# Kernel tuning notes

Hardware: AMD Instinct MI355X
Metric: run time of the kernel (lower is better)

The kernel has to match this reference:

```python
import jax, jax.numpy as jnp
import numpy as np

B, N, DIM = 4, 4096, 768
H = 12
DH = DIM // H          # 64
S = 16                 # num_segments
M = N // S             # 256 segment_len
SCALE = DH ** -0.5


def setup_inputs() -> dict:
    key = jax.random.key(0)
    ks = jax.random.split(key, 7)
    std = DIM ** -0.5
    return {
        "x": jax.random.normal(ks[0], (B, N, DIM), dtype=jnp.float32),
        "Wq": jax.random.normal(ks[1], (DIM, DIM), dtype=jnp.float32) * std,
        "Wkv": jax.random.normal(ks[2], (DIM, DIM), dtype=jnp.float32) * std,
        "Wo": jax.random.normal(ks[3], (DIM, DIM), dtype=jnp.float32) * std,
        "bo": jax.random.normal(ks[4], (DIM,), dtype=jnp.float32) * 0.02,
        "Wo0": jax.random.normal(ks[5], (DIM, DIM), dtype=jnp.float32) * std,
        "bo0": jax.random.normal(ks[6], (DIM,), dtype=jnp.float32) * 0.02,
    }


def _rotary_freqs(n, dh, dtype):
    # lucidrains RotaryEmbedding: inv_freq over even dims, emb = cat(freqs, freqs)
    inv_freq = 1.0 / (10000.0 ** (jnp.arange(0, dh, 2, dtype=jnp.float32) / dh))
    t = jnp.arange(n, dtype=jnp.float32)
    freqs = jnp.einsum("n,f->nf", t, inv_freq)           # (n, dh/2)
    return jnp.concatenate([freqs, freqs], axis=-1).astype(dtype)  # (n, dh)


def _rotate_half(t):
    # '... (j d) -> ... j d', j=2 ; (-x2, x1)
    x1, x2 = jnp.split(t, 2, axis=-1)
    return jnp.concatenate([-x2, x1], axis=-1)


def _apply_rotary(freqs, t):
    # freqs: (1, n, dh) broadcast over (bh, n, dh); rot_dim == dh here
    return t * jnp.cos(freqs) + _rotate_half(t) * jnp.sin(freqs)


def reference(x, Wq, Wkv, Wo, bo, Wo0, bo0):
    b, n, dim = x.shape
    q = x @ Wq            # (b, n, dim), bias-free
    kv = x @ Wkv          # shared K==V projection

    def to_heads(t):      # 'b n (h d) -> (b h) n d'
        return t.reshape(b, n, H, DH).transpose(0, 2, 1, 3).reshape(b * H, n, DH)

    q, kv = to_heads(q), to_heads(kv)

    freqs = _rotary_freqs(n, DH, x.dtype)[None, :, :]    # (1, n, dh)
    q = _apply_rotary(freqs, q)
    kv = _apply_rotary(freqs, kv)

    q = q * SCALE
    c = b * H
    qs = q.reshape(c, S, M, DH)
    kvs = kv.reshape(c, S, M, DH)

    # adjacent-segment KV windows: segment t attends to [t-1, t] for t>=1
    kvs_ccs = jnp.concatenate([kvs[:, :-1], kvs[:, 1:]], axis=2)  # (c, S-1, 2M, dh)
    qs_ccs = qs[:, 1:]                                            # (c, S-1, M, dh)

    lsim = jnp.einsum("csmd,csnd->csmn", qs_ccs, kvs_ccs)         # (c, S-1, M, 2M)
    attn1 = jax.nn.softmax(lsim, axis=-1)
    out1 = jnp.einsum("csmn,csnd->csmd", attn1, kvs_ccs)          # (c, S-1, M, dh)

    # global (self) attention within first segment
    q0, kv0 = qs[:, 0], kvs[:, 0]                                 # (c, M, dh)
    sim0 = jnp.einsum("cmd,cnd->cmn", q0, kv0)
    attn0 = jax.nn.softmax(sim0, axis=-1)
    out0 = jnp.einsum("cmn,cnd->cmd", attn0, kv0)                 # (c, M, dh)

    def merge_heads(t, nn):  # '(b h) nn d -> b nn (h d)'
        return t.reshape(b, H, nn, DH).transpose(0, 2, 1, 3).reshape(b, nn, H * DH)

    out_1 = merge_heads(out1.reshape(c, (S - 1) * M, DH), (S - 1) * M)
    out_0 = merge_heads(out0, M)

    out_1o = out_1 @ Wo + bo
    out_0o = out_0 @ Wo0 + bo0
    return jnp.concatenate([out_0o, out_1o], axis=1)              # (b, n, dim)
```

## Files before the change

kernel.cpp:

```cpp
#include <hip/hip_runtime.h>
#include <hip/hip_bf16.h>


typedef float f32x4 __attribute__((ext_vector_type(4)));
typedef short bf16x8 __attribute__((ext_vector_type(8)));

#define DEV static __device__ __forceinline__

DEV short f2bf(float f) {
  union { __hip_bfloat16 h; unsigned short u; } cv;
  cv.h = __float2bfloat16(f);
  return (short)cv.u;
}

DEV f32x4 fz4() { f32x4 z = {0.f, 0.f, 0.f, 0.f}; return z; }

DEV void gload16(const void* g, void* l) {
  __builtin_amdgcn_global_load_lds((const __attribute__((address_space(1))) void*)g,
                                   (__attribute__((address_space(3))) void*)l, 16, 0, 0);
}

__global__ void __launch_bounds__(256) k_rope(float* __restrict__ cosT,
                                              float* __restrict__ sinT) {
  int idx = blockIdx.x * 256 + threadIdx.x;
  int pos = idx >> 5, jm = idx & 31;
  float invf = exp2f(-(float)jm * (13.287712379549449f / 32.0f));
  float th = (float)pos * invf;
  cosT[idx] = cosf(th);
  sinT[idx] = sinf(th);
}

__global__ void __launch_bounds__(256) k_cvtx(const float* __restrict__ x,
                                              short* __restrict__ xb) {
  int i = (blockIdx.x * 256 + threadIdx.x) * 8;
  float4 a = *(const float4*)(x + i);
  float4 b = *(const float4*)(x + i + 4);
  bf16x8 v;
  v[0] = f2bf(a.x); v[1] = f2bf(a.y); v[2] = f2bf(a.z); v[3] = f2bf(a.w);
  v[4] = f2bf(b.x); v[5] = f2bf(b.y); v[6] = f2bf(b.z); v[7] = f2bf(b.w);
  *(bf16x8*)(xb + i) = v;
}

__global__ void __launch_bounds__(256) k_transw(const float* __restrict__ Wq,
                                                const float* __restrict__ Wkv,
                                                const float* __restrict__ Wo,
                                                const float* __restrict__ Wo0,
                                                short* __restrict__ WtQKV,
                                                short* __restrict__ WtO) {
  __shared__ float t[64][65];
  int z = blockIdx.z;
  const float* src = (z == 0) ? Wq : (z == 1) ? Wkv : (z == 2) ? Wo : Wo0;
  short* dst = (z < 2) ? (WtQKV + (size_t)z * (768 * 768))
                       : (WtO + (size_t)(z - 2) * (768 * 768));
  int k0 = blockIdx.x * 64, j0 = blockIdx.y * 64;
  int tc = threadIdx.x & 63, tr = threadIdx.x >> 6;
#pragma unroll
  for (int i = 0; i < 16; i++) {
    int r = i * 4 + tr;
    t[tc][r] = src[(size_t)(k0 + r) * 768 + j0 + tc];
  }
  __syncthreads();
#pragma unroll
  for (int i = 0; i < 16; i++) {
    int r = i * 4 + tr;
    dst[(size_t)(j0 + r) * 768 + k0 + tc] = f2bf(t[r][tc]);
  }
}

#define QSTAGE(Abuf, Bbuf, Abase, Bbase, kt)                                   \
  {                                                                            \
    _Pragma("unroll") for (int i = 0; i < 2; i++) {                            \
      int rowi = i * 64 + wid * 16 + (lane >> 2);                              \
      int cci = (kt) * 64 + ((((lane & 3) ^ (rowi & 3)) << 4));                \
      gload16((Abase) + (size_t)(r0 + rowi) * 1536 + cci,                      \
              (char*)(Abuf) + i * 4096 + wid * 1024);                          \
      gload16((Bbase) + (size_t)(j0 + rowi) * 1536 + cci,                      \
              (char*)(Bbuf) + i * 4096 + wid * 1024);                          \
    }                                                                          \
  }

__global__ void __launch_bounds__(256, 4) k_gemm_qkv(
    const short* __restrict__ xb, const short* __restrict__ Wt,
    const float* __restrict__ cosT, const float* __restrict__ sinT,
    short* __restrict__ Qb, short* __restrict__ KVb) {
  __shared__ short Al[2][4096];
  __shared__ short Bl[2][4096];
  int bid = blockIdx.x;
  int xcd = bid & 7, loc = bid >> 3;
  int r0 = (xcd * 16 + loc / 12) * 128;
  int cbk = loc % 12;
  bool isQ = cbk < 6;
  int cbl = isQ ? cbk : cbk - 6;
  const char* Ab = (const char*)xb;
  const char* Bb = (const char*)(Wt + (isQ ? (size_t)0 : (size_t)(768 * 768)));
  int j0 = cbl * 128;
  int tid = threadIdx.x, lane = tid & 63, wid = tid >> 6;
  int wr = wid >> 1, wc = wid & 1;
  int l15 = lane & 15, lg = lane >> 4;
  int rsw = (l15 & 3) << 4;

  f32x4 acc[4][4];
#pragma unroll
  for (int i = 0; i < 4; i++)
#pragma unroll
    for (int j = 0; j < 4; j++) acc[i][j] = fz4();

  QSTAGE(Al[0], Bl[0], Ab, Bb, 0)
  for (int kt = 0; kt < 24; kt++) {
    int cb = kt & 1;
    __syncthreads();
    if (kt + 1 < 24) QSTAGE(Al[cb ^ 1], Bl[cb ^ 1], Ab, Bb, kt + 1)
    const char* Ac = (const char*)Al[cb];
    const char* Bc = (const char*)Bl[cb];
    bf16x8 af[4], bfr[4];
#pragma unroll
    for (int mr = 0; mr < 4; mr++)
      af[mr] = *(const bf16x8*)(Ac + (wr * 64 + mr * 16 + l15) * 64 + ((lg * 16) ^ rsw));
#pragma unroll
    for (int nc = 0; nc < 4; nc++)
      bfr[nc] = *(const bf16x8*)(Bc + (wc * 64 + nc * 16 + l15) * 64 + ((lg * 16) ^ rsw));
#pragma unroll
    for (int mr = 0; mr < 4; mr++)
#pragma unroll
      for (int nc = 0; nc < 4; nc++)
        acc[mr][nc] = __builtin_amdgcn_mfma_f32_16x16x32_bf16(af[mr], bfr[nc], acc[mr][nc], 0, 0, 0);
  }

  int h = 2 * cbl + wc;
  short* Ob = isQ ? Qb : KVb;
  float scl = isQ ? 0.18033688011112042f : 1.0f;
#pragma unroll
  for (int mr = 0; mr < 4; mr++) {
#pragma unroll
    for (int rg = 0; rg < 4; rg++) {
      int r = r0 + wr * 64 + mr * 16 + lg * 4 + rg;
      int b = r >> 12, pos = r & 4095;
      const float* cT = cosT + pos * 32;
      const float* sT = sinT + pos * 32;
      float c0 = cT[l15], s0 = sT[l15];
      float c1 = cT[16 + l15], s1 = sT[16 + l15];
      float v0 = acc[mr][0][rg], v1 = acc[mr][1][rg];
      float v2 = acc[mr][2][rg], v3 = acc[mr][3][rg];
      size_t base = ((size_t)((b * 12 + h) * 4096 + pos)) * 64 + l15;
      Ob[base]      = f2bf((v0 * c0 - v2 * s0) * scl);
      Ob[base + 16] = f2bf((v1 * c1 - v3 * s1) * scl);
      Ob[base + 32] = f2bf((v2 * c0 + v0 * s0) * scl);
      Ob[base + 48] = f2bf((v3 * c1 + v1 * s1) * scl);
    }
  }
}

__global__ void __launch_bounds__(256) k_transkv(const short* __restrict__ KVb,
                                                 short* __restrict__ KVt) {
  __shared__ short T[64][72];
  int c = blockIdx.x;
  int pt = blockIdx.y;
  int t = threadIdx.x;
  int ch = t & 7, rr = t >> 3;
#pragma unroll
  for (int i = 0; i < 2; i++) {
    int p = rr + i * 32;
    bf16x8 v = *(const bf16x8*)&KVb[((size_t)c * 4096 + pt * 64 + p) * 64 + ch * 8];
    *(bf16x8*)&T[p][ch * 8] = v;
  }
  __syncthreads();
#pragma unroll
  for (int i = 0; i < 2; i++) {
    int d = rr + i * 32;
    bf16x8 v;
#pragma unroll
    for (int j = 0; j < 8; j++) {
      int cc = ch * 8 + j;
      int g = cc >> 5, sig = cc & 31;
      int p = g * 32 + 4 * (sig >> 3) + (sig & 3) + 16 * ((sig >> 2) & 1);
      v[j] = T[p][d];
    }
    *(bf16x8*)&KVt[((size_t)c * 64 + d) * 4096 + pt * 64 + ch * 8] = v;
  }
}

#define STAGE(buf, kk0)                                                        \
  {                                                                            \
    _Pragma("unroll") for (int i = 0; i < 2; i++) {                            \
      gload16(KVc + (size_t)((kk0) + i * 32 + krow) * 128 + ksrccol,           \
              (char*)Kl[buf] + i * 4096 + wid * 1024);                         \
      gload16(KVtc + ((size_t)(i * 32 + krow) * 4096 + (kk0)) * 2 + ksrccol,   \
              (char*)Vl[buf] + i * 4096 + wid * 1024);                         \
    }                                                                          \
  }

__global__ void __launch_bounds__(256, 4) k_attn(const short* __restrict__ Qb,
                                                 const short* __restrict__ KVbp,
                                                 const short* __restrict__ KVtp,
                                                 short* __restrict__ AO) {
  __shared__ short Kl[2][4096];
  __shared__ short Vl[2][4096];
  int bid = blockIdx.x;
  int orig = (bid & 7) * 192 + (bid >> 3);
  int c = orig >> 5;
  int e = orig & 31;
  int s = (e < 2) ? 0 : ((e - 2) >> 1) + 1;
  int qh = (e < 2) ? e : (e - 2) & 1;
  int NC = (s == 0) ? 4 : 8;
  int Kbase = (s == 0) ? 0 : (s - 1) * 256;

  int tid = threadIdx.x, lane = tid & 63, wid = tid >> 6;
  int l15 = lane & 15, lg = lane >> 4;
  const char* KVc = (const char*)(KVbp + (size_t)c * 4096 * 64);
  const char* KVtc = (const char*)(KVtp + (size_t)c * 64 * 4096);

  int krow = tid >> 3;
  int ksrccol = ((tid & 7) * 16) ^ ((krow & 7) << 4);
  int swz = (l15 & 7) << 4;

  int q0 = s * 256 + qh * 128 + wid * 32;
  bf16x8 qf[2][2];
#pragma unroll
  for (int qt = 0; qt < 2; qt++) {
    const short* Qr = Qb + ((size_t)c * 4096 + q0 + qt * 16 + l15) * 64 + lg * 8;
    qf[qt][0] = *(const bf16x8*)Qr;
    qf[qt][1] = *(const bf16x8*)(Qr + 32);
  }

  const f32x4 mi = {-32.f, -32.f, -32.f, -32.f};
  bf16x8 ones;
#pragma unroll
  for (int j = 0; j < 8; j++) ones[j] = (short)0x3F80;

  f32x4 oacc[2][4];
  f32x4 lacc[2];
#pragma unroll
  for (int qt = 0; qt < 2; qt++) {
    lacc[qt] = fz4();
#pragma unroll
    for (int vt = 0; vt < 4; vt++) oacc[qt][vt] = fz4();
  }

  STAGE(0, Kbase)
  for (int ch = 0; ch < NC; ch++) {
    int cb = ch & 1;
    __syncthreads();
    if (ch + 1 < NC) STAGE(cb ^ 1, Kbase + (ch + 1) * 64)
    const char* Kb_ = (const char*)Kl[cb];
    const char* Vb_ = (const char*)Vl[cb];
#pragma unroll
    for (int u = 0; u < 2; u++) {
      f32x4 z[2][2];
#pragma unroll
      for (int t2 = 0; t2 < 2; t2++) {
        const char* Kp = Kb_ + ((2 * u + t2) * 16 + l15) * 128;
        bf16x8 kf0 = *(const bf16x8*)(Kp + ((lg * 16) ^ swz));
        bf16x8 kf1 = *(const bf16x8*)(Kp + ((64 + lg * 16) ^ swz));
        __builtin_amdgcn_s_setprio(1);
#pragma unroll
        for (int qt = 0; qt < 2; qt++) {
          f32x4 zz = __builtin_amdgcn_mfma_f32_16x16x32_bf16(kf0, qf[qt][0], mi, 0, 0, 0);
          zz = __builtin_amdgcn_mfma_f32_16x16x32_bf16(kf1, qf[qt][1], zz, 0, 0, 0);
          z[qt][t2] = zz;
        }
        __builtin_amdgcn_s_setprio(0);
      }
      bf16x8 pf[2];
#pragma unroll
      for (int qt = 0; qt < 2; qt++) {
#pragma unroll
        for (int t2 = 0; t2 < 2; t2++)
#pragma unroll
          for (int r = 0; r < 4; r++)
            pf[qt][t2 * 4 + r] = f2bf(exp2f(z[qt][t2][r]));
      }
      bf16x8 vf[4];
#pragma unroll
      for (int vt = 0; vt < 4; vt++)
        vf[vt] = *(const bf16x8*)(Vb_ + (vt * 16 + l15) * 128 +
                                  ((u * 64 + lg * 16) ^ swz));
      __builtin_amdgcn_s_setprio(1);
#pragma unroll
      for (int qt = 0; qt < 2; qt++) {
#pragma unroll
        for (int vt = 0; vt < 4; vt++)
          oacc[qt][vt] = __builtin_amdgcn_mfma_f32_16x16x32_bf16(pf[qt], vf[vt], oacc[qt][vt], 0, 0, 0);
        lacc[qt] = __builtin_amdgcn_mfma_f32_16x16x32_bf16(pf[qt], ones, lacc[qt], 0, 0, 0);
      }
      __builtin_amdgcn_s_setprio(0);
    }
  }

  int bq = c / 12, hh = c % 12;
#pragma unroll
  for (int qt = 0; qt < 2; qt++) {
    float rinv[4];
#pragma unroll
    for (int r = 0; r < 4; r++) rinv[r] = 1.0f / lacc[qt][r];
#pragma unroll
    for (int vt = 0; vt < 4; vt++)
#pragma unroll
      for (int r = 0; r < 4; r++) {
        size_t row = (size_t)bq * 4096 + q0 + qt * 16 + lg * 4 + r;
        AO[row * 768 + hh * 64 + vt * 16 + l15] = f2bf(oacc[qt][vt][r] * rinv[r]);
      }
  }
}

__global__ void __launch_bounds__(256, 4) k_gemm_out(
    const short* __restrict__ AO, const short* __restrict__ Wt,
    const float* __restrict__ bo, const float* __restrict__ bo0,
    float* __restrict__ out) {
  __shared__ short Al[2][4096];
  __shared__ short Bl[2][4096];
  int bid = blockIdx.x;
  int xcd = bid & 7, loc = bid >> 3;
  int r0 = (xcd * 16 + loc / 6) * 128;
  int j0 = (loc % 6) * 128;
  bool o0sel = (r0 & 4095) < 256;
  const char* Ab = (const char*)AO;
  const char* Bb = (const char*)(Wt + (o0sel ? (size_t)1 : (size_t)0) * (768 * 768));
  const float* bias = o0sel ? bo0 : bo;
  int tid = threadIdx.x, lane = tid & 63, wid = tid >> 6;
  int wr = wid >> 1, wc = wid & 1;
  int l15 = lane & 15, lg = lane >> 4;
  int rsw = (l15 & 3) << 4;

  f32x4 acc[4][4];
#pragma unroll
  for (int i = 0; i < 4; i++)
#pragma unroll
    for (int j = 0; j < 4; j++) acc[i][j] = fz4();

  QSTAGE(Al[0], Bl[0], Ab, Bb, 0)
  for (int kt = 0; kt < 24; kt++) {
    int cb = kt & 1;
    __syncthreads();
    if (kt + 1 < 24) QSTAGE(Al[cb ^ 1], Bl[cb ^ 1], Ab, Bb, kt + 1)
    const char* Ac = (const char*)Al[cb];
    const char* Bc = (const char*)Bl[cb];
    bf16x8 af[4], bfr[4];
#pragma unroll
    for (int mr = 0; mr < 4; mr++)
      af[mr] = *(const bf16x8*)(Ac + (wr * 64 + mr * 16 + l15) * 64 + ((lg * 16) ^ rsw));
#pragma unroll
    for (int nc = 0; nc < 4; nc++)
      bfr[nc] = *(const bf16x8*)(Bc + (wc * 64 + nc * 16 + l15) * 64 + ((lg * 16) ^ rsw));
#pragma unroll
    for (int mr = 0; mr < 4; mr++)
#pragma unroll
      for (int nc = 0; nc < 4; nc++)
        acc[mr][nc] = __builtin_amdgcn_mfma_f32_16x16x32_bf16(af[mr], bfr[nc], acc[mr][nc], 0, 0, 0);
  }

  float bs[4];
#pragma unroll
  for (int nc = 0; nc < 4; nc++) bs[nc] = bias[j0 + wc * 64 + nc * 16 + l15];
#pragma unroll
  for (int mr = 0; mr < 4; mr++)
#pragma unroll
    for (int rg = 0; rg < 4; rg++) {
      size_t r = (size_t)r0 + wr * 64 + mr * 16 + lg * 4 + rg;
      float* op = out + r * 768 + j0 + wc * 64 + l15;
      op[0]  = acc[mr][0][rg] + bs[0];
      op[16] = acc[mr][1][rg] + bs[1];
      op[32] = acc[mr][2][rg] + bs[2];
      op[48] = acc[mr][3][rg] + bs[3];
    }
}

extern "C" void kernel_launch(void* const* d_in, const int* in_sizes, int n_in,
                              void* d_out, int out_size, void* d_ws, size_t ws_size,
                              hipStream_t stream) {
  (void)in_sizes; (void)n_in; (void)out_size; (void)ws_size;
  const float* x   = (const float*)d_in[0];
  const float* Wq  = (const float*)d_in[1];
  const float* Wkv = (const float*)d_in[2];
  const float* Wo  = (const float*)d_in[3];
  const float* bo  = (const float*)d_in[4];
  const float* Wo0 = (const float*)d_in[5];
  const float* bo0 = (const float*)d_in[6];
  float* out = (float*)d_out;

  char* ws = (char*)d_ws;
  short* xb    = (short*)(ws + 0);
  short* AO    = xb;
  short* Qb    = (short*)(ws + 25165824);
  short* KVb   = (short*)(ws + 50331648);
  short* KVt   = (short*)(ws + 75497472);
  short* WtQKV = (short*)(ws + 75497472);
  float* cosT  = (float*)(ws + 77856768);
  float* sinT  = (float*)(ws + 78381056);
  short* WtO   = (short*)(ws + 100663296);

  k_rope<<<512, 256, 0, stream>>>(cosT, sinT);
  k_cvtx<<<6144, 256, 0, stream>>>(x, xb);
  k_transw<<<dim3(12, 12, 4), 256, 0, stream>>>(Wq, Wkv, Wo, Wo0, WtQKV, WtO);
  k_gemm_qkv<<<1536, 256, 0, stream>>>(xb, WtQKV, cosT, sinT, Qb, KVb);
  k_transkv<<<dim3(48, 64), 256, 0, stream>>>(KVb, KVt);
  k_attn<<<1536, 256, 0, stream>>>(Qb, KVb, KVt, AO);
  k_gemm_out<<<768, 256, 0, stream>>>(AO, WtO, bo, bo0, out);
}
```

Measured before the change: 156.5 us.

## Use a four-stage LDS ring with explicit vmcnt waits in projection GEMMs

Replaces the double-buffered k-loop in the QKV and output projection GEMMs with a 4-slot shared-memory ring that prefetches two k-steps ahead. It uses explicit s_waitcnt vmcnt counts and a raw s_barrier instead of __syncthreads. The goal is to hide global-to-LDS load latency behind MFMA work. In exchange, LDS use rises to 64KB per block and launch bounds drop from 4 to 2 blocks per CU, which lowers occupancy.

```diff
diff --git a/kernel.cpp b/kernel.cpp
--- a/kernel.cpp
+++ b/kernel.cpp
@@ -67,24 +67,55 @@
   }
 }
 
-#define QSTAGE(Abuf, Bbuf, Abase, Bbase, kt)                                   \
+#define STAGE32(Lbuf, Abase, Bbase, s)                                         \
   {                                                                            \
     _Pragma("unroll") for (int i = 0; i < 2; i++) {                            \
-      int rowi = i * 64 + wid * 16 + (lane >> 2);                              \
-      int cci = (kt) * 64 + ((((lane & 3) ^ (rowi & 3)) << 4));                \
-      gload16((Abase) + (size_t)(r0 + rowi) * 1536 + cci,                      \
-              (char*)(Abuf) + i * 4096 + wid * 1024);                          \
-      gload16((Bbase) + (size_t)(j0 + rowi) * 1536 + cci,                      \
-              (char*)(Bbuf) + i * 4096 + wid * 1024);                          \
+      int ch_ = i * 256 + tid;                                                 \
+      int row_ = ch_ >> 2, c_ = ch_ & 3;                                       \
+      int col_ = (s) * 64 + ((c_ ^ (row_ & 3)) << 4);                          \
+      gload16((Abase) + (size_t)(r0 + row_) * 1536 + col_,                     \
+              (char*)(Lbuf) + i * 4096 + wid * 1024);                          \
+      gload16((Bbase) + (size_t)(j0 + row_) * 1536 + col_,                     \
+              (char*)(Lbuf) + 8192 + i * 4096 + wid * 1024);                   \
     }                                                                          \
   }
 
-__global__ void __launch_bounds__(256, 4) k_gemm_qkv(
+#define RING_KLOOP(LQ, Ab, Bb, BODY)                                           \
+  STAGE32(LQ[0], Ab, Bb, 0)                                                    \
+  STAGE32(LQ[1], Ab, Bb, 1)                                                    \
+  for (int s = 0; s < 24; s++) {                                               \
+    if (s < 22) {                                                              \
+      STAGE32(LQ[(s + 2) & 3], Ab, Bb, s + 2)                                  \
+      asm volatile("s_waitcnt vmcnt(8)" ::: "memory");                         \
+    } else if (s == 22) {                                                      \
+      asm volatile("s_waitcnt vmcnt(4)" ::: "memory");                         \
+    } else {                                                                   \
+      asm volatile("s_waitcnt vmcnt(0)" ::: "memory");                         \
+    }                                                                          \
+    __builtin_amdgcn_sched_barrier(0);                                         \
+    __builtin_amdgcn_s_barrier();                                              \
+    __builtin_amdgcn_sched_barrier(0);                                         \
+    const char* Ac = (const char*)LQ[s & 3];                                   \
+    const char* Bc = Ac + 8192;                                                \
+    bf16x8 af[4], bfr[4];                                                      \
+    _Pragma("unroll") for (int mr = 0; mr < 4; mr++)                           \
+        af[mr] = *(const bf16x8*)(Ac + (wr * 64 + mr * 16 + l15) * 64 + rsw);  \
+    _Pragma("unroll") for (int nc = 0; nc < 4; nc++)                           \
+        bfr[nc] = *(const bf16x8*)(Bc + (wc * 64 + nc * 16 + l15) * 64 + rsw); \
+    BODY                                                                       \
+  }
+
+#define MFMA16                                                                 \
+  _Pragma("unroll") for (int mr = 0; mr < 4; mr++)                             \
+      _Pragma("unroll") for (int nc = 0; nc < 4; nc++)                         \
+          acc[mr][nc] = __builtin_amdgcn_mfma_f32_16x16x32_bf16(               \
+              af[mr], bfr[nc], acc[mr][nc], 0, 0, 0);
+
+__global__ void __launch_bounds__(256, 2) k_gemm_qkv(
     const short* __restrict__ xb, const short* __restrict__ Wt,
     const float* __restrict__ cosT, const float* __restrict__ sinT,
     short* __restrict__ Qb, short* __restrict__ KVb) {
-  __shared__ short Al[2][4096];
-  __shared__ short Bl[2][4096];
+  __shared__ char Lq[4][16384];
   int bid = blockIdx.x;
   int xcd = bid & 7, loc = bid >> 3;
   int r0 = (xcd * 16 + loc / 12) * 128;
@@ -97,7 +128,7 @@
   int tid = threadIdx.x, lane = tid & 63, wid = tid >> 6;
   int wr = wid >> 1, wc = wid & 1;
   int l15 = lane & 15, lg = lane >> 4;
-  int rsw = (l15 & 3) << 4;
+  int rsw = ((lg ^ (l15 & 3)) << 4);
 
   f32x4 acc[4][4];
 #pragma unroll
@@ -105,26 +136,7 @@
 #pragma unroll
     for (int j = 0; j < 4; j++) acc[i][j] = fz4();
 
-  QSTAGE(Al[0], Bl[0], Ab, Bb, 0)
-  for (int kt = 0; kt < 24; kt++) {
-    int cb = kt & 1;
-    __syncthreads();
-    if (kt + 1 < 24) QSTAGE(Al[cb ^ 1], Bl[cb ^ 1], Ab, Bb, kt + 1)
-    const char* Ac = (const char*)Al[cb];
-    const char* Bc = (const char*)Bl[cb];
-    bf16x8 af[4], bfr[4];
-#pragma unroll
-    for (int mr = 0; mr < 4; mr++)
-      af[mr] = *(const bf16x8*)(Ac + (wr * 64 + mr * 16 + l15) * 64 + ((lg * 16) ^ rsw));
-#pragma unroll
-    for (int nc = 0; nc < 4; nc++)
-      bfr[nc] = *(const bf16x8*)(Bc + (wc * 64 + nc * 16 + l15) * 64 + ((lg * 16) ^ rsw));
-#pragma unroll
-    for (int mr = 0; mr < 4; mr++)
-#pragma unroll
-      for (int nc = 0; nc < 4; nc++)
-        acc[mr][nc] = __builtin_amdgcn_mfma_f32_16x16x32_bf16(af[mr], bfr[nc], acc[mr][nc], 0, 0, 0);
-  }
+  RING_KLOOP(Lq, Ab, Bb, MFMA16)
 
   int h = 2 * cbl + wc;
   short* Ob = isQ ? Qb : KVb;
@@ -302,12 +314,11 @@
   }
 }
 
-__global__ void __launch_bounds__(256, 4) k_gemm_out(
+__global__ void __launch_bounds__(256, 2) k_gemm_out(
     const short* __restrict__ AO, const short* __restrict__ Wt,
     const float* __restrict__ bo, const float* __restrict__ bo0,
     float* __restrict__ out) {
-  __shared__ short Al[2][4096];
-  __shared__ short Bl[2][4096];
+  __shared__ char Lq[4][16384];
   int bid = blockIdx.x;
   int xcd = bid & 7, loc = bid >> 3;
   int r0 = (xcd * 16 + loc / 6) * 128;
@@ -319,7 +330,7 @@
   int tid = threadIdx.x, lane = tid & 63, wid = tid >> 6;
   int wr = wid >> 1, wc = wid & 1;
   int l15 = lane & 15, lg = lane >> 4;
-  int rsw = (l15 & 3) << 4;
+  int rsw = ((lg ^ (l15 & 3)) << 4);
 
   f32x4 acc[4][4];
 #pragma unroll
@@ -327,26 +338,7 @@
 #pragma unroll
     for (int j = 0; j < 4; j++) acc[i][j] = fz4();
 
-  QSTAGE(Al[0], Bl[0], Ab, Bb, 0)
-  for (int kt = 0; kt < 24; kt++) {
-    int cb = kt & 1;
-    __syncthreads();
-    if (kt + 1 < 24) QSTAGE(Al[cb ^ 1], Bl[cb ^ 1], Ab, Bb, kt + 1)
-    const char* Ac = (const char*)Al[cb];
-    const char* Bc = (const char*)Bl[cb];
-    bf16x8 af[4], bfr[4];
-#pragma unroll
-    for (int mr = 0; mr < 4; mr++)
-      af[mr] = *(const bf16x8*)(Ac + (wr * 64 + mr * 16 + l15) * 64 + ((lg * 16) ^ rsw));
-#pragma unroll
-    for (int nc = 0; nc < 4; nc++)
-      bfr[nc] = *(const bf16x8*)(Bc + (wc * 64 + nc * 16 + l15) * 64 + ((lg * 16) ^ rsw));
-#pragma unroll
-    for (int mr = 0; mr < 4; mr++)
-#pragma unroll
-      for (int nc = 0; nc < 4; nc++)
-        acc[mr][nc] = __builtin_amdgcn_mfma_f32_16x16x32_bf16(af[mr], bfr[nc], acc[mr][nc], 0, 0, 0);
-  }
+  RING_KLOOP(Lq, Ab, Bb, MFMA16)
 
   float bs[4];
 #pragma unroll
```

After: 157.0 us. About the same (+0.3%).
